# Kernel optimization log

Measured on AMD Instinct MI355X. Metric: run time of the kernel, lower is better.

The kernel has to match this reference:

```python
import jax, jax.numpy as jnp
import numpy as np

N = 500_000      # total nodes in batched graph
B = 2_048        # number of graphs (segments)
D = 256          # input_dim == hidden_dim == output_dim


def setup_inputs() -> dict:
    key = jax.random.key(0)
    k = jax.random.split(key, 8)
    feat = jax.random.normal(k[0], (N, D), dtype=jnp.float32)
    cnt = jax.random.uniform(k[1], (N,), dtype=jnp.float32)
    segment_ids = jnp.sort(jax.random.randint(k[2], (N,), 0, B, dtype=jnp.int32))
    last_nodes = jax.random.randint(k[3], (B,), 0, N, dtype=jnp.int32)
    # learned parameters (torch nn.Linear: y = x @ W.T + b)
    s = 1.0 / np.sqrt(D)
    W_u = jax.random.uniform(k[4], (D, D), dtype=jnp.float32, minval=-s, maxval=s)
    W_v = jax.random.uniform(k[5], (D, D), dtype=jnp.float32, minval=-s, maxval=s)
    b_v = jax.random.uniform(k[6], (D,), dtype=jnp.float32, minval=-s, maxval=s)
    w_e = jax.random.uniform(k[7], (D,), dtype=jnp.float32, minval=-s, maxval=s)
    return {"feat": feat, "cnt": cnt, "segment_ids": segment_ids,
            "last_nodes": last_nodes, "W_u": W_u, "W_v": W_v,
            "b_v": b_v, "w_e": w_e}


def reference(feat, cnt, segment_ids, last_nodes, W_u, W_v, b_v, w_e):
    # fc_u: per-node projection  [N, D]
    feat_u = feat @ W_u.T
    # fc_v on last node of each graph, then broadcast back to nodes
    feat_v = feat[last_nodes] @ W_v.T + b_v          # [B, D]
    feat_vb = feat_v[segment_ids]                    # [N, D] broadcast_nodes
    # fc_e(sigmoid(u + v)) -> scalar gate per node
    e = jax.nn.sigmoid(feat_u + feat_vb) @ w_e       # [N]
    alpha = e * cnt                                  # [N]
    # segment-sum readout over graphs
    rst = jax.ops.segment_sum(feat * alpha[:, None], segment_ids,
                              num_segments=B)        # [B, D]
    return rst
```

## Files before the change

kernel.cpp:

```cpp
#include <hip/hip_runtime.h>
#include <hip/hip_bf16.h>

typedef __attribute__((ext_vector_type(8))) short short8;
typedef __attribute__((ext_vector_type(4))) float f32x4;

#define D 256
#define MT 64
#define NW 8
#define GRID_MAIN 256
#define GV 16

__device__ __forceinline__ unsigned pack2(float a, float b) {
    __hip_bfloat162 hh = __float22bfloat162_rn(make_float2(a, b));
    return *(unsigned*)&hh;
}
__device__ __forceinline__ float fast_sigmoid(float x) {
    return __builtin_amdgcn_rcpf(1.f + __expf(-x));
}
__device__ __forceinline__ void dma16(const void* g, void* lds) {
    __builtin_amdgcn_global_load_lds((const __attribute__((address_space(1))) unsigned int*)g,
                                     (__attribute__((address_space(3))) unsigned int*)lds, 16, 0, 0);
}
__device__ __forceinline__ void dma4(const void* g, void* lds) {
    __builtin_amdgcn_global_load_lds((const __attribute__((address_space(1))) unsigned int*)g,
                                     (__attribute__((address_space(3))) unsigned int*)lds, 4, 0, 0);
}

__global__ __launch_bounds__(256) void k_prep(
    const float* __restrict__ feat, const int* __restrict__ last_nodes,
    const float* __restrict__ Wv, const float* __restrict__ bv,
    const float* __restrict__ Wu, unsigned short* __restrict__ Wub,
    float* __restrict__ featv, float* __restrict__ rst, int Bseg, int nOut) {
    const int b = blockIdx.x;
    const int t = threadIdx.x;
    if (b < 128) {
        __shared__ float fln[GV][D];
        const int b0 = b * GV;
        for (int g = 0; g < GV; ++g) {
            int bb = b0 + g;
            int ln = (bb < Bseg) ? last_nodes[bb] : 0;
            fln[g][t] = feat[(long)ln * D + t];
        }
        __syncthreads();
        float acc[GV];
        float bvj = bv[t];
        #pragma unroll
        for (int g = 0; g < GV; ++g) acc[g] = bvj;
        const float* wr = Wv + (long)t * D;
        for (int k = 0; k < D; k += 4) {
            float4 w4 = *(const float4*)(wr + k);
            #pragma unroll
            for (int g = 0; g < GV; ++g) {
                acc[g] += w4.x * fln[g][k]     + w4.y * fln[g][k + 1]
                        + w4.z * fln[g][k + 2] + w4.w * fln[g][k + 3];
            }
        }
        for (int g = 0; g < GV; ++g)
            if (b0 + g < Bseg) featv[(long)(b0 + g) * D + t] = acc[g];
    } else if (b < 384) {
        int i = (b - 128) * 256 + t;
        if (i < D * D) Wub[i] = (unsigned short)(pack2(Wu[i], 0.f) & 0xffffu);
    } else {
        int base = (b - 384) * 1024 + t;
        #pragma unroll
        for (int it = 0; it < 4; ++it) {
            int i = base + it * 256;
            if (i < nOut) rst[i] = 0.f;
        }
    }
}

__global__ __launch_bounds__(512, 2) void k_main(
    const float* __restrict__ feat, const float* __restrict__ cnt,
    const int* __restrict__ seg, const unsigned short* __restrict__ Wub,
    const float* __restrict__ featv, const float* __restrict__ we,
    float* __restrict__ rst, int N) {

    __shared__ float stageF[MT][D];
    __shared__ unsigned short Abuf[2][MT][D];
    __shared__ int   seg_s[4][MT];
    __shared__ float cnt_s[4][MT];
    __shared__ float e_s[NW][MT];
    __shared__ float alpha_s[MT];

    const int t  = threadIdx.x;
    const int w  = t >> 6;
    const int l  = t & 63;
    const int rl = l & 15;
    const int h  = l >> 4;

    const int T   = (N + MT - 1) / MT;
    const int nb  = gridDim.x;
    const int per = T / nb, rem = T % nb;
    const int bid = blockIdx.x;
    const int c0  = bid * per + (bid < rem ? bid : rem);
    const int c1  = c0 + per + (bid < rem ? 1 : 0);
    if (c0 >= c1) return;

#define STAGE(ti)                                                             \
    {                                                                         \
        const long nb0 = (long)(ti) * MT;                                     \
        long nsx = nb0 + l; if (nsx > (long)N - 1) nsx = (long)N - 1;         \
        dma4(seg + nsx, &seg_s[(ti) & 3][0]);                                 \
        dma4(cnt + nsx, &cnt_s[(ti) & 3][0]);                                 \
        asm volatile("" ::: "memory");                                        \
        _Pragma("unroll")                                                     \
        for (int i = 0; i < 8; ++i) {                                         \
            int r = w + 8 * i;                                                \
            long nn = nb0 + r; if (nn > (long)N - 1) nn = (long)N - 1;        \
            dma16(feat + nn * D + 4 * l, &stageF[r][0]);                      \
        }                                                                     \
    }

#define CONVERT(buf)                                                          \
    {                                                                         \
        _Pragma("unroll")                                                     \
        for (int i = 0; i < 8; ++i) {                                         \
            int r = w + 8 * i;                                                \
            f32x4 fv = *(const f32x4*)&stageF[r][4 * l];                      \
            *(uint2*)&Abuf[buf][r][(((l >> 1) ^ (r & 7)) << 3) + ((l & 1) << 2)] = \
                make_uint2(pack2(fv[0], fv[1]), pack2(fv[2], fv[3]));         \
        }                                                                     \
    }

    short8 a_reg[2][8];
    {
        const unsigned short* ab = Wub + (long)(32 * w + rl) * D + h * 8;
        #pragma unroll
        for (int mt = 0; mt < 2; ++mt)
            #pragma unroll
            for (int s = 0; s < 8; ++s)
                a_reg[mt][s] = *(const short8*)(ab + (long)mt * 16 * D + s * 32);
    }
    f32x4 wev[2];
    wev[0] = *(const f32x4*)(we + 32 * w + h * 4);
    wev[1] = *(const f32x4*)(we + 32 * w + 16 + h * 4);

    f32x4 fvr[2][4];
    STAGE(c0);
    asm volatile("s_waitcnt vmcnt(0)" ::: "memory");
    CONVERT(c0 & 1);
    {
        #pragma unroll
        for (int nt = 0; nt < 4; ++nt) {
            int sg = seg_s[c0 & 3][nt * 16 + rl];
            const float* fb = featv + (long)sg * D + 32 * w + h * 4;
            fvr[0][nt] = *(const f32x4*)(fb);
            fvr[1][nt] = *(const f32x4*)(fb + 16);
        }
    }
    asm volatile("" ::: "memory");
    if (c0 + 1 < c1) STAGE(c0 + 1);
    asm volatile("s_waitcnt lgkmcnt(0)\ns_barrier" ::: "memory");

    for (int tt = c0; tt < c1; ++tt) {
        const long n0 = (long)tt * MT;
        const bool more1 = (tt + 1 < c1);
        const bool more2 = (tt + 2 < c1);
        const int  cur   = tt & 1;
        const int* seg_t = seg_s[tt & 3];

        if (more1) asm volatile("s_waitcnt vmcnt(8)" ::: "memory");
        else       asm volatile("s_waitcnt vmcnt(0)" ::: "memory");

        f32x4 acc[2][4];
        #pragma unroll
        for (int mt = 0; mt < 2; ++mt)
            #pragma unroll
            for (int nt = 0; nt < 4; ++nt) acc[mt][nt] = (f32x4)0.f;

        const unsigned short* Ab = &Abuf[cur][0][0];
        #pragma unroll
        for (int s = 0; s < 8; ++s) {
            short8 bfr[4];
            #pragma unroll
            for (int nt = 0; nt < 4; ++nt) {
                int R  = nt * 16 + rl;
                int gr = (s * 4 + h) ^ (rl & 7);
                bfr[nt] = *(const short8*)(Ab + R * D + gr * 8);
            }
            #pragma unroll
            for (int mt = 0; mt < 2; ++mt)
                #pragma unroll
                for (int nt = 0; nt < 4; ++nt)
                    acc[mt][nt] = __builtin_amdgcn_mfma_f32_16x16x32_bf16(a_reg[mt][s], bfr[nt], acc[mt][nt], 0, 0, 0);
        }

        float ep[4] = {0.f, 0.f, 0.f, 0.f};
        #pragma unroll
        for (int mt = 0; mt < 2; ++mt)
            #pragma unroll
            for (int nt = 0; nt < 4; ++nt)
                #pragma unroll
                for (int r = 0; r < 4; ++r)
                    ep[nt] += wev[mt][r] * fast_sigmoid(acc[mt][nt][r] + fvr[mt][nt][r]);
        #pragma unroll
        for (int nt = 0; nt < 4; ++nt) {
            ep[nt] += __shfl_xor(ep[nt], 16);
            ep[nt] += __shfl_xor(ep[nt], 32);
        }
        if (h == 0) {
            #pragma unroll
            for (int nt = 0; nt < 4; ++nt) e_s[w][nt * 16 + rl] = ep[nt];
        }
        asm volatile("s_waitcnt lgkmcnt(0)\ns_barrier" ::: "memory");

        if (t < MT) {
            float e = 0.f;
            #pragma unroll
            for (int q = 0; q < NW; ++q) e += e_s[q][t];
            alpha_s[t] = (n0 + t < N) ? e * cnt_s[tt & 3][t] : 0.f;
        }
        asm volatile("s_waitcnt lgkmcnt(0)\ns_barrier" ::: "memory");

        if (more1) {
            const int* sn = seg_s[(tt + 1) & 3];
            #pragma unroll
            for (int nt = 0; nt < 4; ++nt) {
                int sg = sn[nt * 16 + rl];
                const float* fb = featv + (long)sg * D + 32 * w + h * 4;
                fvr[0][nt] = *(const f32x4*)(fb);
                fvr[1][nt] = *(const f32x4*)(fb + 16);
            }
            asm volatile("" ::: "memory");
        }

        long rb_p = -1; float ca_p = 0.f, cb_p = 0.f;
        {
            const int p   = t & 127;
            const int gq  = t >> 7;
            const int i0  = gq * 16;
            const int nv  = (int)(((long)N - n0 < MT) ? ((long)N - n0) : MT);
            const int i1  = (i0 + 16 < nv) ? (i0 + 16) : nv;
            const unsigned* Ab32 = (const unsigned*)Ab;
            if (i0 < i1) {
                if ((i1 - i0) == 16 && seg_t[i0] == seg_t[i1 - 1]) {
                    float ca = 0.f, cb = 0.f, ca2 = 0.f, cb2 = 0.f;
                    #pragma unroll
                    for (int i2 = 0; i2 < 16; i2 += 2) {
                        int i = i0 + i2;
                        unsigned v0 = Ab32[(i + 0) * 128 + (((p >> 2) ^ ((i + 0) & 7)) << 2) + (p & 3)];
                        unsigned v1 = Ab32[(i + 1) * 128 + (((p >> 2) ^ ((i + 1) & 7)) << 2) + (p & 3)];
                        float a0 = alpha_s[i + 0], a1 = alpha_s[i + 1];
                        ca  += __uint_as_float(v0 << 16) * a0;
                        cb  += __uint_as_float(v0 & 0xffff0000u) * a0;
                        ca2 += __uint_as_float(v1 << 16) * a1;
                        cb2 += __uint_as_float(v1 & 0xffff0000u) * a1;
                    }
                    rb_p = (long)seg_t[i0] * D + 2 * p;
                    ca_p = ca + ca2; cb_p = cb + cb2;
                } else {
                    float ca = 0.f, cb = 0.f;
                    int curseg = seg_t[i0];
                    for (int i = i0; i < i1; ++i) {
                        int sgi = seg_t[i];
                        if (sgi != curseg) {
                            long rb = (long)curseg * D + 2 * p;
                            atomicAdd(&rst[rb], ca); atomicAdd(&rst[rb + 1], cb);
                            ca = cb = 0.f; curseg = sgi;
                        }
                        unsigned v = Ab32[i * 128 + (((p >> 2) ^ (i & 7)) << 2) + (p & 3)];
                        float al = alpha_s[i];
                        ca += __uint_as_float(v << 16) * al;
                        cb += __uint_as_float(v & 0xffff0000u) * al;
                    }
                    rb_p = (long)curseg * D + 2 * p;
                    ca_p = ca; cb_p = cb;
                }
            }
        }
        asm volatile("" ::: "memory");

        if (more1) {
            asm volatile("s_waitcnt vmcnt(0)" ::: "memory");
            CONVERT((tt + 1) & 1);
        }

        if (rb_p >= 0) {
            atomicAdd(&rst[rb_p], ca_p);
            atomicAdd(&rst[rb_p + 1], cb_p);
        }
        asm volatile("" ::: "memory");

        if (more2) {
            STAGE(tt + 2);
            asm volatile("" ::: "memory");
        }

        asm volatile("s_waitcnt lgkmcnt(0)\ns_barrier" ::: "memory");
    }
#undef STAGE
#undef CONVERT
}

extern "C" void kernel_launch(void* const* d_in, const int* in_sizes, int n_in,
                              void* d_out, int out_size, void* d_ws, size_t ws_size,
                              hipStream_t stream) {
    const float* feat = (const float*)d_in[0];
    const float* cnt  = (const float*)d_in[1];
    const int*   segp = (const int*)d_in[2];
    const int*   last = (const int*)d_in[3];
    const float* Wu   = (const float*)d_in[4];
    const float* Wv   = (const float*)d_in[5];
    const float* bv   = (const float*)d_in[6];
    const float* we   = (const float*)d_in[7];
    float* rst = (float*)d_out;

    const int N    = in_sizes[1];
    const int Bseg = in_sizes[3];

    unsigned short* Wub   = (unsigned short*)d_ws;
    float*          featv = (float*)((char*)d_ws + (size_t)D * D * sizeof(unsigned short));

    const int zero_blocks = (out_size + 1023) / 1024;
    k_prep<<<384 + zero_blocks, 256, 0, stream>>>(feat, last, Wv, bv, Wu, Wub, featv, rst, Bseg, out_size);
    k_main<<<GRID_MAIN, 512, 0, stream>>>(feat, cnt, segp, Wub, featv, we, rst, N);
}
```

Before: 192.0 us.

## Restructure main loop pipeline, reduce alpha via LDS atomics, drop a barrier

Moves the conversion of the next tile and the staging of the tile after it to just after the MFMA block, so those loads overlap the sigmoid and segment-sum work. The per-node gate is now summed with LDS atomicAdd into a double-buffered alpha array instead of an e_s scratch plus a separate reduction pass, which removes one barrier per tile. It also raises wave priority around the MFMA loop. In exchange there is a full vmcnt(0) wait right after the MFMA, extra LDS atomic contention, and the featv row loads move to the end of the loop where their latency is less hidden.

```diff
diff --git a/kernel.cpp b/kernel.cpp
--- a/kernel.cpp
+++ b/kernel.cpp
@@ -9,6 +9,8 @@
 #define NW 8
 #define GRID_MAIN 256
 #define GV 16
+
+#define BAR_LGKM asm volatile("s_waitcnt lgkmcnt(0)\ns_barrier" ::: "memory")
 
 __device__ __forceinline__ unsigned pack2(float a, float b) {
     __hip_bfloat162 hh = __float22bfloat162_rn(make_float2(a, b));
@@ -80,8 +82,7 @@
     __shared__ unsigned short Abuf[2][MT][D];
     __shared__ int   seg_s[4][MT];
     __shared__ float cnt_s[4][MT];
-    __shared__ float e_s[NW][MT];
-    __shared__ float alpha_s[MT];
+    __shared__ float alpha_s[2][MT];
 
     const int t  = threadIdx.x;
     const int w  = t >> 6;
@@ -140,6 +141,9 @@
     STAGE(c0);
     asm volatile("s_waitcnt vmcnt(0)" ::: "memory");
     CONVERT(c0 & 1);
+    asm volatile("s_waitcnt lgkmcnt(0)" ::: "memory");
+    if (c0 + 1 < c1) STAGE(c0 + 1);
+    if (t < 2 * MT) ((float*)alpha_s)[t] = 0.f;
     {
         #pragma unroll
         for (int nt = 0; nt < 4; ++nt) {
@@ -149,9 +153,7 @@
             fvr[1][nt] = *(const f32x4*)(fb + 16);
         }
     }
-    asm volatile("" ::: "memory");
-    if (c0 + 1 < c1) STAGE(c0 + 1);
-    asm volatile("s_waitcnt lgkmcnt(0)\ns_barrier" ::: "memory");
+    BAR_LGKM;
 
     for (int tt = c0; tt < c1; ++tt) {
         const long n0 = (long)tt * MT;
@@ -160,9 +162,6 @@
         const int  cur   = tt & 1;
         const int* seg_t = seg_s[tt & 3];
 
-        if (more1) asm volatile("s_waitcnt vmcnt(8)" ::: "memory");
-        else       asm volatile("s_waitcnt vmcnt(0)" ::: "memory");
-
         f32x4 acc[2][4];
         #pragma unroll
         for (int mt = 0; mt < 2; ++mt)
@@ -170,6 +169,7 @@
             for (int nt = 0; nt < 4; ++nt) acc[mt][nt] = (f32x4)0.f;
 
         const unsigned short* Ab = &Abuf[cur][0][0];
+        __builtin_amdgcn_s_setprio(1);
         #pragma unroll
         for (int s = 0; s < 8; ++s) {
             short8 bfr[4];
@@ -185,6 +185,18 @@
                 for (int nt = 0; nt < 4; ++nt)
                     acc[mt][nt] = __builtin_amdgcn_mfma_f32_16x16x32_bf16(a_reg[mt][s], bfr[nt], acc[mt][nt], 0, 0, 0);
         }
+        __builtin_amdgcn_s_setprio(0);
+
+        if (more1) asm volatile("s_waitcnt vmcnt(0)" ::: "memory");
+
+        if (more1) {
+            CONVERT((tt + 1) & 1);
+            asm volatile("s_waitcnt lgkmcnt(0)" ::: "memory");
+        }
+        if (more2) {
+            STAGE(tt + 2);
+            asm volatile("" ::: "memory");
+        }
 
         float ep[4] = {0.f, 0.f, 0.f, 0.f};
         #pragma unroll
@@ -201,29 +213,15 @@
         }
         if (h == 0) {
             #pragma unroll
-            for (int nt = 0; nt < 4; ++nt) e_s[w][nt * 16 + rl] = ep[nt];
-        }
-        asm volatile("s_waitcnt lgkmcnt(0)\ns_barrier" ::: "memory");
-
-        if (t < MT) {
-            float e = 0.f;
-            #pragma unroll
-            for (int q = 0; q < NW; ++q) e += e_s[q][t];
-            alpha_s[t] = (n0 + t < N) ? e * cnt_s[tt & 3][t] : 0.f;
-        }
-        asm volatile("s_waitcnt lgkmcnt(0)\ns_barrier" ::: "memory");
-
-        if (more1) {
-            const int* sn = seg_s[(tt + 1) & 3];
-            #pragma unroll
             for (int nt = 0; nt < 4; ++nt) {
-                int sg = sn[nt * 16 + rl];
-                const float* fb = featv + (long)sg * D + 32 * w + h * 4;
-                fvr[0][nt] = *(const f32x4*)(fb);
-                fvr[1][nt] = *(const f32x4*)(fb + 16);
-            }
-            asm volatile("" ::: "memory");
-        }
+                int node = nt * 16 + rl;
+                if (n0 + node < N)
+                    atomicAdd(&alpha_s[cur][node], ep[nt] * cnt_s[tt & 3][node]);
+            }
+        }
+        BAR_LGKM;
+
+        if (t < MT) alpha_s[cur ^ 1][t] = 0.f;
 
         long rb_p = -1; float ca_p = 0.f, cb_p = 0.f;
         {
@@ -233,6 +231,7 @@
             const int nv  = (int)(((long)N - n0 < MT) ? ((long)N - n0) : MT);
             const int i1  = (i0 + 16 < nv) ? (i0 + 16) : nv;
             const unsigned* Ab32 = (const unsigned*)Ab;
+            const float* al_s = alpha_s[cur];
             if (i0 < i1) {
                 if ((i1 - i0) == 16 && seg_t[i0] == seg_t[i1 - 1]) {
                     float ca = 0.f, cb = 0.f, ca2 = 0.f, cb2 = 0.f;
@@ -241,7 +240,7 @@
                         int i = i0 + i2;
                         unsigned v0 = Ab32[(i + 0) * 128 + (((p >> 2) ^ ((i + 0) & 7)) << 2) + (p & 3)];
                         unsigned v1 = Ab32[(i + 1) * 128 + (((p >> 2) ^ ((i + 1) & 7)) << 2) + (p & 3)];
-                        float a0 = alpha_s[i + 0], a1 = alpha_s[i + 1];
+                        float a0 = al_s[i + 0], a1 = al_s[i + 1];
                         ca  += __uint_as_float(v0 << 16) * a0;
                         cb  += __uint_as_float(v0 & 0xffff0000u) * a0;
                         ca2 += __uint_as_float(v1 << 16) * a1;
@@ -260,7 +259,7 @@
                             ca = cb = 0.f; curseg = sgi;
                         }
                         unsigned v = Ab32[i * 128 + (((p >> 2) ^ (i & 7)) << 2) + (p & 3)];
-                        float al = alpha_s[i];
+                        float al = al_s[i];
                         ca += __uint_as_float(v << 16) * al;
                         cb += __uint_as_float(v & 0xffff0000u) * al;
                     }
@@ -269,25 +268,24 @@
                 }
             }
         }
-        asm volatile("" ::: "memory");
-
-        if (more1) {
-            asm volatile("s_waitcnt vmcnt(0)" ::: "memory");
-            CONVERT((tt + 1) & 1);
-        }
-
         if (rb_p >= 0) {
             atomicAdd(&rst[rb_p], ca_p);
             atomicAdd(&rst[rb_p + 1], cb_p);
         }
         asm volatile("" ::: "memory");
 
-        if (more2) {
-            STAGE(tt + 2);
+        if (more1) {
+            const int* sn = seg_s[(tt + 1) & 3];
+            #pragma unroll
+            for (int nt = 0; nt < 4; ++nt) {
+                int sg = sn[nt * 16 + rl];
+                const float* fb = featv + (long)sg * D + 32 * w + h * 4;
+                fvr[0][nt] = *(const f32x4*)(fb);
+                fvr[1][nt] = *(const f32x4*)(fb + 16);
+            }
             asm volatile("" ::: "memory");
         }
-
-        asm volatile("s_waitcnt lgkmcnt(0)\ns_barrier" ::: "memory");
+        BAR_LGKM;
     }
 #undef STAGE
 #undef CONVERT
```

Result: slower. 215.3 us (+12.1%).

## Shrink node tile to 32 with 4 waves, each wave owning 64 output columns

Applied to the files above, without the earlier changes.

Halves the node tile (MT 64→32) and block size (512→256 threads, 4 waves), doubles the grid to 512 blocks, and gives each wave 64 hidden columns (4 MFMA m-tiles) with W_u held in registers. It also raises wave priority around the MFMA loop, and moves the gather of next-tile featv rows to after the CONVERT step. The goal is a smaller LDS footprint per block, more resident blocks, and a shorter per-tile critical path. The cost is doubled register use for a_reg, which may limit occupancy, and more barriers per node processed.

```diff
diff --git a/kernel.cpp b/kernel.cpp
--- a/kernel.cpp
+++ b/kernel.cpp
@@ -5,10 +5,12 @@
 typedef __attribute__((ext_vector_type(4))) float f32x4;
 
 #define D 256
-#define MT 64
-#define NW 8
-#define GRID_MAIN 256
+#define MT 32
+#define NW 4
+#define GRID_MAIN 512
 #define GV 16
+
+#define BAR_LGKM asm volatile("s_waitcnt lgkmcnt(0)\ns_barrier" ::: "memory")
 
 __device__ __forceinline__ unsigned pack2(float a, float b) {
     __hip_bfloat162 hh = __float22bfloat162_rn(make_float2(a, b));
@@ -70,7 +72,7 @@
     }
 }
 
-__global__ __launch_bounds__(512, 2) void k_main(
+__global__ __launch_bounds__(256, 2) void k_main(
     const float* __restrict__ feat, const float* __restrict__ cnt,
     const int* __restrict__ seg, const unsigned short* __restrict__ Wub,
     const float* __restrict__ featv, const float* __restrict__ we,
@@ -78,8 +80,8 @@
 
     __shared__ float stageF[MT][D];
     __shared__ unsigned short Abuf[2][MT][D];
-    __shared__ int   seg_s[4][MT];
-    __shared__ float cnt_s[4][MT];
+    __shared__ int   seg_s[4][64];
+    __shared__ float cnt_s[4][64];
     __shared__ float e_s[NW][MT];
     __shared__ float alpha_s[MT];
 
@@ -106,7 +108,7 @@
         asm volatile("" ::: "memory");                                        \
         _Pragma("unroll")                                                     \
         for (int i = 0; i < 8; ++i) {                                         \
-            int r = w + 8 * i;                                                \
+            int r = w + 4 * i;                                                \
             long nn = nb0 + r; if (nn > (long)N - 1) nn = (long)N - 1;        \
             dma16(feat + nn * D + 4 * l, &stageF[r][0]);                      \
         }                                                                     \
@@ -116,42 +118,44 @@
     {                                                                         \
         _Pragma("unroll")                                                     \
         for (int i = 0; i < 8; ++i) {                                         \
-            int r = w + 8 * i;                                                \
+            int r = w + 4 * i;                                                \
             f32x4 fv = *(const f32x4*)&stageF[r][4 * l];                      \
             *(uint2*)&Abuf[buf][r][(((l >> 1) ^ (r & 7)) << 3) + ((l & 1) << 2)] = \
                 make_uint2(pack2(fv[0], fv[1]), pack2(fv[2], fv[3]));         \
         }                                                                     \
     }
 
-    short8 a_reg[2][8];
+    short8 a_reg[4][8];
     {
-        const unsigned short* ab = Wub + (long)(32 * w + rl) * D + h * 8;
-        #pragma unroll
-        for (int mt = 0; mt < 2; ++mt)
+        const unsigned short* ab = Wub + (long)(64 * w + rl) * D + h * 8;
+        #pragma unroll
+        for (int mt = 0; mt < 4; ++mt)
             #pragma unroll
             for (int s = 0; s < 8; ++s)
                 a_reg[mt][s] = *(const short8*)(ab + (long)mt * 16 * D + s * 32);
     }
-    f32x4 wev[2];
-    wev[0] = *(const f32x4*)(we + 32 * w + h * 4);
-    wev[1] = *(const f32x4*)(we + 32 * w + 16 + h * 4);
+    f32x4 wev[4];
+    #pragma unroll
+    for (int mt = 0; mt < 4; ++mt)
+        wev[mt] = *(const f32x4*)(we + 64 * w + 16 * mt + 4 * h);
 
     f32x4 fvr[2][4];
     STAGE(c0);
     asm volatile("s_waitcnt vmcnt(0)" ::: "memory");
     CONVERT(c0 & 1);
+    asm volatile("s_waitcnt lgkmcnt(0)" ::: "memory");
     {
         #pragma unroll
-        for (int nt = 0; nt < 4; ++nt) {
+        for (int nt = 0; nt < 2; ++nt) {
             int sg = seg_s[c0 & 3][nt * 16 + rl];
-            const float* fb = featv + (long)sg * D + 32 * w + h * 4;
-            fvr[0][nt] = *(const f32x4*)(fb);
-            fvr[1][nt] = *(const f32x4*)(fb + 16);
+            const float* fb = featv + (long)sg * D + 64 * w + 4 * h;
+            #pragma unroll
+            for (int mt = 0; mt < 4; ++mt) fvr[nt][mt] = *(const f32x4*)(fb + 16 * mt);
         }
     }
     asm volatile("" ::: "memory");
     if (c0 + 1 < c1) STAGE(c0 + 1);
-    asm volatile("s_waitcnt lgkmcnt(0)\ns_barrier" ::: "memory");
+    BAR_LGKM;
 
     for (int tt = c0; tt < c1; ++tt) {
         const long n0 = (long)tt * MT;
@@ -160,70 +164,50 @@
         const int  cur   = tt & 1;
         const int* seg_t = seg_s[tt & 3];
 
-        if (more1) asm volatile("s_waitcnt vmcnt(8)" ::: "memory");
-        else       asm volatile("s_waitcnt vmcnt(0)" ::: "memory");
-
-        f32x4 acc[2][4];
-        #pragma unroll
-        for (int mt = 0; mt < 2; ++mt)
-            #pragma unroll
-            for (int nt = 0; nt < 4; ++nt) acc[mt][nt] = (f32x4)0.f;
+        f32x4 acc[4][2];
+        #pragma unroll
+        for (int mt = 0; mt < 4; ++mt)
+            #pragma unroll
+            for (int nt = 0; nt < 2; ++nt) acc[mt][nt] = (f32x4)0.f;
 
         const unsigned short* Ab = &Abuf[cur][0][0];
+        __builtin_amdgcn_s_setprio(1);
         #pragma unroll
         for (int s = 0; s < 8; ++s) {
-            short8 bfr[4];
-            #pragma unroll
-            for (int nt = 0; nt < 4; ++nt) {
+            short8 bfr[2];
+            #pragma unroll
+            for (int nt = 0; nt < 2; ++nt) {
                 int R  = nt * 16 + rl;
                 int gr = (s * 4 + h) ^ (rl & 7);
                 bfr[nt] = *(const short8*)(Ab + R * D + gr * 8);
             }
             #pragma unroll
-            for (int mt = 0; mt < 2; ++mt)
+            for (int mt = 0; mt < 4; ++mt)
                 #pragma unroll
-                for (int nt = 0; nt < 4; ++nt)
+                for (int nt = 0; nt < 2; ++nt)
                     acc[mt][nt] = __builtin_amdgcn_mfma_f32_16x16x32_bf16(a_reg[mt][s], bfr[nt], acc[mt][nt], 0, 0, 0);
         }
-
-        float ep[4] = {0.f, 0.f, 0.f, 0.f};
-        #pragma unroll
-        for (int mt = 0; mt < 2; ++mt)
-            #pragma unroll
-            for (int nt = 0; nt < 4; ++nt)
+        __builtin_amdgcn_s_setprio(0);
+
+        #pragma unroll
+        for (int nt = 0; nt < 2; ++nt) {
+            float ep = 0.f;
+            #pragma unroll
+            for (int mt = 0; mt < 4; ++mt)
                 #pragma unroll
                 for (int r = 0; r < 4; ++r)
-                    ep[nt] += wev[mt][r] * fast_sigmoid(acc[mt][nt][r] + fvr[mt][nt][r]);
-        #pragma unroll
-        for (int nt = 0; nt < 4; ++nt) {
-            ep[nt] += __shfl_xor(ep[nt], 16);
-            ep[nt] += __shfl_xor(ep[nt], 32);
-        }
-        if (h == 0) {
-            #pragma unroll
-            for (int nt = 0; nt < 4; ++nt) e_s[w][nt * 16 + rl] = ep[nt];
-        }
-        asm volatile("s_waitcnt lgkmcnt(0)\ns_barrier" ::: "memory");
+                    ep += wev[mt][r] * fast_sigmoid(acc[mt][nt][r] + fvr[nt][mt][r]);
+            ep += __shfl_xor(ep, 16);
+            ep += __shfl_xor(ep, 32);
+            if (h == 0) e_s[w][nt * 16 + rl] = ep;
+        }
+        BAR_LGKM;
 
         if (t < MT) {
-            float e = 0.f;
-            #pragma unroll
-            for (int q = 0; q < NW; ++q) e += e_s[q][t];
+            float e = e_s[0][t] + e_s[1][t] + e_s[2][t] + e_s[3][t];
             alpha_s[t] = (n0 + t < N) ? e * cnt_s[tt & 3][t] : 0.f;
         }
-        asm volatile("s_waitcnt lgkmcnt(0)\ns_barrier" ::: "memory");
-
-        if (more1) {
-            const int* sn = seg_s[(tt + 1) & 3];
-            #pragma unroll
-            for (int nt = 0; nt < 4; ++nt) {
-                int sg = sn[nt * 16 + rl];
-                const float* fb = featv + (long)sg * D + 32 * w + h * 4;
-                fvr[0][nt] = *(const f32x4*)(fb);
-                fvr[1][nt] = *(const f32x4*)(fb + 16);
-            }
-            asm volatile("" ::: "memory");
-        }
+        BAR_LGKM;
 
         long rb_p = -1; float ca_p = 0.f, cb_p = 0.f;
         {
@@ -274,6 +258,19 @@
         if (more1) {
             asm volatile("s_waitcnt vmcnt(0)" ::: "memory");
             CONVERT((tt + 1) & 1);
+            asm volatile("s_waitcnt lgkmcnt(0)" ::: "memory");
+        }
+
+        if (more1) {
+            const int* sn = seg_s[(tt + 1) & 3];
+            #pragma unroll
+            for (int nt = 0; nt < 2; ++nt) {
+                int sg = sn[nt * 16 + rl];
+                const float* fb = featv + (long)sg * D + 64 * w + 4 * h;
+                #pragma unroll
+                for (int mt = 0; mt < 4; ++mt) fvr[nt][mt] = *(const f32x4*)(fb + 16 * mt);
+            }
+            asm volatile("" ::: "memory");
         }
 
         if (rb_p >= 0) {
@@ -286,8 +283,7 @@
             STAGE(tt + 2);
             asm volatile("" ::: "memory");
         }
-
-        asm volatile("s_waitcnt lgkmcnt(0)\ns_barrier" ::: "memory");
+        BAR_LGKM;
     }
 #undef STAGE
 #undef CONVERT
@@ -314,5 +310,5 @@
 
     const int zero_blocks = (out_size + 1023) / 1024;
     k_prep<<<384 + zero_blocks, 256, 0, stream>>>(feat, last, Wv, bv, Wu, Wub, featv, rst, Bseg, out_size);
-    k_main<<<GRID_MAIN, 512, 0, stream>>>(feat, cnt, segp, Wub, featv, we, rst, N);
-}
+    k_main<<<GRID_MAIN, 256, 0, stream>>>(feat, cnt, segp, Wub, featv, we, rst, N);
+}
```

New measurement: 383.1 us. +99.5%, slower.
